# Optimization experiments

Measured on AMD Instinct MI355X. Metric: run time of the kernel, lower is better.

Reference implementation:

```python
import jax, jax.numpy as jnp
import numpy as np

# Module hyper-parameters (match init_kwargs)
WIN = 64        # windowSize -> N
REC = 128       # receptiveSize -> M
H = 8           # numHeads
D = 32          # headDim
DIM = 256       # dim
MAXD = WIN + (REC - WIN) // 2  # maxDisparity = 96

# Static relative position index table, shape (N, M), values in [0, 2*MAXD)
_coords_x = np.arange(WIN)[:, None]
_coords_x_ = (np.arange(REC) - (REC - WIN) // 2)[None, :]
REL_IDX = jnp.asarray(_coords_x - _coords_x_ + MAXD, dtype=jnp.int32)


def setup_inputs() -> dict:
    key = jax.random.key(0)
    ks = jax.random.split(key, 12)
    B, nW = 4, 256
    B_ = B * nW
    x = jax.random.normal(ks[0], (B_, WIN, DIM), jnp.float32)
    x_ = jax.random.normal(ks[1], (B_, REC, DIM), jnp.float32)
    mask_left = jax.random.randint(ks[2], (2, WIN, REC), 0, 2, jnp.int32)
    mask_right = jax.random.randint(ks[3], (2, WIN, REC), 0, 2, jnp.int32)
    s = 0.02
    q_w = jax.random.normal(ks[4], (DIM, H * D), jnp.float32) * s
    q_b = jnp.zeros((H * D,), jnp.float32)
    kv_w = jax.random.normal(ks[5], (DIM, 2 * H * D), jnp.float32) * s
    kv_b = jnp.zeros((2 * H * D,), jnp.float32)
    proj_w = jax.random.normal(ks[6], (H * D, DIM), jnp.float32) * s
    proj_b = jnp.zeros((DIM,), jnp.float32)
    bias_table = jax.random.normal(ks[7], (2 * MAXD, H), jnp.float32) * s
    return dict(x=x, x_=x_, mask_left=mask_left, mask_right=mask_right, nW=nW,
                q_w=q_w, q_b=q_b, kv_w=kv_w, kv_b=kv_b,
                proj_w=proj_w, proj_b=proj_b, bias_table=bias_table)


def reference(x, x_, mask_left, mask_right, nW, q_w, q_b, kv_w, kv_b, proj_w, proj_b, bias_table):
    B_, N, C = x.shape
    M = x_.shape[1]
    B = B_ // nW
    scale = D ** -0.5

    q = (x @ q_w + q_b).reshape(B_, N, H, D).transpose(0, 2, 1, 3)   # b h n d
    kv = x_ @ kv_w + kv_b
    k, v = jnp.split(kv, 2, axis=-1)
    k = k.reshape(B_, M, H, D).transpose(0, 2, 1, 3)                 # b h m d
    v = v.reshape(B_, M, H, D).transpose(0, 2, 1, 3)                 # b h m d

    attn = jnp.einsum('bhnd,bhmd->bhnm', q, k) * scale
    # gathered relative position bias: (N, M, H) -> (H, N, M)
    bias = bias_table[REL_IDX].transpose(2, 0, 1)
    attn = attn + bias[None]

    mask_value = -jnp.finfo(attn.dtype).max
    attn = attn.reshape(B, nW, H, N, M)
    mc = min(mask_left.shape[0], nW)  # static python int
    ml = (mask_left[:mc] == 1)[None, :, None]        # (1, mc, 1, N, M)
    attn = attn.at[:, :mc].set(jnp.where(ml, mask_value, attn[:, :mc]))
    mr = (mask_right[mask_right.shape[0] - mc:] == 1)[None, :, None]
    attn = attn.at[:, nW - mc:].set(jnp.where(mr, mask_value, attn[:, nW - mc:]))
    attn = attn.reshape(B_, H, N, M)

    attn = jax.nn.softmax(attn, axis=-1)
    out = jnp.einsum('bhnm,bhmd->bhnd', attn, v)
    out = out.transpose(0, 2, 1, 3).reshape(B_, N, H * D)
    out = out @ proj_w + proj_b
    return out
```

## Files before the change

### kernel.cpp

```cpp
#include <hip/hip_runtime.h>
#include <float.h>


typedef __attribute__((ext_vector_type(8))) short bf16x8;
typedef __attribute__((ext_vector_type(4))) float f32x4;

static __device__ __forceinline__ unsigned int f2bf(float f) {
    unsigned int u = __float_as_uint(f);
    return (u + 0x7FFFu + ((u >> 16) & 1u)) >> 16;
}
static __device__ __forceinline__ unsigned int pack2(float lo, float hi) {
    return f2bf(lo) | (f2bf(hi) << 16);
}

__device__ unsigned short g_Wt[262144];

__global__ __launch_bounds__(256) void prep_wt(
    const float* __restrict__ q_w, const float* __restrict__ kv_w, const float* __restrict__ proj_w)
{
    const int b = blockIdx.x, k = threadIdx.x;
    float v; unsigned short* dst;
    if (b < 256)      { v = q_w[k * 256 + b];            dst = g_Wt + b * 256; }
    else if (b < 768) { v = kv_w[k * 512 + (b - 256)];   dst = g_Wt + 65536 + (b - 256) * 256; }
    else              { v = proj_w[k * 256 + (b - 768)]; dst = g_Wt + 196608 + (b - 768) * 256; }
    dst[k] = (unsigned short)f2bf(v);
}

template<int NC, int WT_OFF, bool ABF16, bool F32OUT>
__global__ __launch_bounds__(512) void gemm_db(
    const void* __restrict__ Ain, const float* __restrict__ bias, void* __restrict__ Cout)
{
    constexpr int NBN = NC / 128;
    __shared__ __align__(16) unsigned short As[2][128 * 64];
    __shared__ __align__(16) unsigned short Ws[2][128 * 64];

    const int nbx = 8 * NBN;
    const int g = blockIdx.x / nbx, r = blockIdx.x % nbx;
    const int bn = r >> 3, bm = g * 8 + (r & 7);
    const size_t r0 = (size_t)bm * 128;
    const int c0 = bn * 128;

    const int t = threadIdx.x;
    const int wave = t >> 6, lane = t & 63;
    const int lr = lane & 15, hi = lane >> 4;
    const int rw = (wave >> 2) * 64, cw = (wave & 3) * 32;
    const int srow = t >> 2, sks = (t & 3) * 16;
    const int aswz = (srow & 7) << 4;
    const int so1 = (2 * sks) ^ aswz, so2 = (2 * sks + 16) ^ aswz;

    f32x4 acc[4][2];
    #pragma unroll
    for (int i = 0; i < 4; ++i)
        #pragma unroll
        for (int j = 0; j < 2; ++j) acc[i][j] = (f32x4){0.f, 0.f, 0.f, 0.f};

    float4 fA0, fA1, fA2, fA3;
    uint4  sA0, sA1;
    uint4  sW0, sW1;

#define STAGE_LOAD(K0)                                                                     \
    {                                                                                      \
        const unsigned short* wsrc = g_Wt + WT_OFF + (size_t)(c0 + srow) * 256 + (K0) + sks; \
        sW0 = *(const uint4*)wsrc; sW1 = *(const uint4*)(wsrc + 8);                        \
        if (ABF16) {                                                                       \
            const unsigned short* asrc = (const unsigned short*)Ain + (r0 + srow) * 256 + (K0) + sks; \
            sA0 = *(const uint4*)asrc; sA1 = *(const uint4*)(asrc + 8);                    \
        } else {                                                                           \
            const float* asrc = (const float*)Ain + (r0 + srow) * 256 + (K0) + sks;        \
            fA0 = *(const float4*)asrc;       fA1 = *(const float4*)(asrc + 4);            \
            fA2 = *(const float4*)(asrc + 8); fA3 = *(const float4*)(asrc + 12);           \
        }                                                                                  \
    }

#define STAGE_WRITE(B)                                                                     \
    {                                                                                      \
        char* ad = (char*)As[B] + srow * 128;                                              \
        char* wd = (char*)Ws[B] + srow * 128;                                              \
        uint4 u0, u1;                                                                      \
        if (ABF16) { u0 = sA0; u1 = sA1; }                                                 \
        else {                                                                             \
            u0 = make_uint4(pack2(fA0.x, fA0.y), pack2(fA0.z, fA0.w),                      \
                            pack2(fA1.x, fA1.y), pack2(fA1.z, fA1.w));                     \
            u1 = make_uint4(pack2(fA2.x, fA2.y), pack2(fA2.z, fA2.w),                      \
                            pack2(fA3.x, fA3.y), pack2(fA3.z, fA3.w));                     \
        }                                                                                  \
        *(uint4*)(ad + so1) = u0; *(uint4*)(ad + so2) = u1;                                \
        *(uint4*)(wd + so1) = sW0; *(uint4*)(wd + so2) = sW1;                              \
    }

#define COMPUTE(B)                                                                         \
    {                                                                                      \
        const char* Ab = (const char*)As[B];                                               \
        const char* Wb = (const char*)Ws[B];                                               \
        const int swzr = (lr & 7) << 4;                                                    \
        _Pragma("unroll")                                                                  \
        for (int kk = 0; kk < 2; ++kk) {                                                   \
            const int ko = (kk * 64 + hi * 16) ^ swzr;                                     \
            bf16x8 af[4], bf[2];                                                           \
            _Pragma("unroll")                                                              \
            for (int i = 0; i < 4; ++i)                                                    \
                af[i] = *(const bf16x8*)(Ab + (rw + i * 16 + lr) * 128 + ko);              \
            _Pragma("unroll")                                                              \
            for (int j = 0; j < 2; ++j)                                                    \
                bf[j] = *(const bf16x8*)(Wb + (cw + j * 16 + lr) * 128 + ko);              \
            _Pragma("unroll")                                                              \
            for (int i = 0; i < 4; ++i)                                                    \
                _Pragma("unroll")                                                          \
                for (int j = 0; j < 2; ++j)                                                \
                    acc[i][j] = __builtin_amdgcn_mfma_f32_16x16x32_bf16(af[i], bf[j], acc[i][j], 0, 0, 0); \
        }                                                                                  \
    }

    STAGE_LOAD(0); STAGE_WRITE(0); __syncthreads();
    STAGE_LOAD(64);
    COMPUTE(0);
    STAGE_WRITE(1);
    STAGE_LOAD(128);
    __syncthreads();
    COMPUTE(1);
    STAGE_WRITE(0);
    STAGE_LOAD(192);
    __syncthreads();
    COMPUTE(0);
    STAGE_WRITE(1);
    __syncthreads();
    COMPUTE(1);

#undef STAGE_LOAD
#undef STAGE_WRITE
#undef COMPUTE

    #pragma unroll
    for (int i = 0; i < 4; ++i) {
        #pragma unroll
        for (int bj = 0; bj < 2; ++bj) {
            const int col = c0 + cw + bj * 16 + lr;
            const float bb = bias[col];
            #pragma unroll
            for (int q = 0; q < 4; ++q) {
                const size_t row = r0 + rw + i * 16 + 4 * hi + q;
                const float val = acc[i][bj][q] + bb;
                if (F32OUT) ((float*)Cout)[row * NC + col] = val;
                else        ((unsigned short*)Cout)[row * NC + col] = (unsigned short)f2bf(val);
            }
        }
    }
}

__global__ __launch_bounds__(256) void attn_fused(
    const unsigned short* __restrict__ qbf, const unsigned short* __restrict__ kvbf,
    const float* __restrict__ bias_table, const int* __restrict__ mask_left,
    const int* __restrict__ mask_right, unsigned short* __restrict__ aout)
{
    __shared__ __align__(16) unsigned short Qn[64 * 32];
    __shared__ __align__(16) unsigned short Kn[128 * 32];
    __shared__ __align__(16) unsigned short Vt[32 * 128];
    __shared__ __align__(16) unsigned short Pn[64 * 128];
    __shared__ float ballT[8 * 192];

    const int w = blockIdx.x;
    const int t = threadIdx.x;
    const int wave = t >> 6, lane = t & 63;
    const int lr = lane & 15, hi = lane >> 4;
    const int n0w = wave * 16;

    for (int i = t; i < 1536; i += 256) {
        const int hh = i / 192, r = i - hh * 192;
        ballT[i] = bias_table[r * 8 + hh];
    }

    const int wi = w & 255;
    const int* mbase = nullptr;
    if (wi < 2) mbase = mask_left + wi * (64 * 128);
    else if (wi >= 254) mbase = mask_right + (wi - 254) * (64 * 128);

    const float scale = 0.17677669529663687f;

    for (int h = 0; h < 8; ++h) {
        __syncthreads();
        {
            const int n = t >> 2, dq = t & 3;
            const uint4 v = *(const uint4*)(qbf + ((size_t)(w * 64 + n)) * 256 + h * 32 + dq * 8);
            *(uint4*)((char*)Qn + n * 64 + dq * 16) = v;
        }
        #pragma unroll
        for (int i = 0; i < 2; ++i) {
            const int m = (t >> 2) + 64 * i, dq = t & 3;
            const uint4 v = *(const uint4*)(kvbf + ((size_t)(w * 128 + m)) * 512 + h * 32 + dq * 8);
            *(uint4*)((char*)Kn + m * 64 + dq * 16) = v;
        }
        #pragma unroll
        for (int i = 0; i < 2; ++i) {
            const int db = (t >> 7) * 2 + i, m = t & 127;
            const uint4 v = *(const uint4*)(kvbf + ((size_t)(w * 128 + m)) * 512 + 256 + h * 32 + db * 8);
            const unsigned short* vs = (const unsigned short*)&v;
            #pragma unroll
            for (int e = 0; e < 8; ++e) {
                const int d = db * 8 + e;
                *(unsigned short*)((char*)Vt + d * 256 + ((2 * m) ^ ((d & 7) << 4))) = vs[e];
            }
        }
        __syncthreads();

        const bf16x8 qa = *(const bf16x8*)((char*)Qn + (n0w + lr) * 64 + 16 * hi);
        f32x4 sacc[8];
        #pragma unroll
        for (int mj = 0; mj < 8; ++mj) {
            sacc[mj] = (f32x4){0.f, 0.f, 0.f, 0.f};
            const bf16x8 kb = *(const bf16x8*)((char*)Kn + (mj * 16 + lr) * 64 + 16 * hi);
            sacc[mj] = __builtin_amdgcn_mfma_f32_16x16x32_bf16(qa, kb, sacc[mj], 0, 0, 0);
        }

        const float* bh = ballT + h * 192;
        #pragma unroll
        for (int mj = 0; mj < 8; ++mj) {
            const int m = 16 * mj + lr;
            #pragma unroll
            for (int q = 0; q < 4; ++q) {
                const int n = n0w + 4 * hi + q;
                sacc[mj][q] = fmaf(sacc[mj][q], scale, bh[n - m + 128]);
            }
        }
        if (mbase) {
            #pragma unroll
            for (int mj = 0; mj < 8; ++mj) {
                const int m = 16 * mj + lr;
                #pragma unroll
                for (int q = 0; q < 4; ++q) {
                    const int n = n0w + 4 * hi + q;
                    if (mbase[n * 128 + m] == 1) sacc[mj][q] = -FLT_MAX;
                }
            }
        }

        float inv[4];
        #pragma unroll
        for (int q = 0; q < 4; ++q) {
            float mx = sacc[0][q];
            #pragma unroll
            for (int mj = 1; mj < 8; ++mj) mx = fmaxf(mx, sacc[mj][q]);
            mx = fmaxf(mx, __shfl_xor(mx, 1));
            mx = fmaxf(mx, __shfl_xor(mx, 2));
            mx = fmaxf(mx, __shfl_xor(mx, 4));
            mx = fmaxf(mx, __shfl_xor(mx, 8));
            float sm = 0.f;
            #pragma unroll
            for (int mj = 0; mj < 8; ++mj) {
                sacc[mj][q] = __expf(sacc[mj][q] - mx);
                sm += sacc[mj][q];
            }
            sm += __shfl_xor(sm, 1);
            sm += __shfl_xor(sm, 2);
            sm += __shfl_xor(sm, 4);
            sm += __shfl_xor(sm, 8);
            inv[q] = 1.0f / sm;
        }

        #pragma unroll
        for (int mj = 0; mj < 8; ++mj) {
            #pragma unroll
            for (int q = 0; q < 4; ++q) {
                const float pv = sacc[mj][q];
                const float po = __shfl_xor(pv, 1);
                if (!(lane & 1)) {
                    const int n = n0w + 4 * hi + q;
                    const int m = 16 * mj + lr;
                    const unsigned int u = f2bf(pv) | (f2bf(po) << 16);
                    *(unsigned int*)((char*)Pn + n * 256 + ((2 * m) ^ ((n & 7) << 4))) = u;
                }
            }
        }

        f32x4 oacc[2];
        oacc[0] = (f32x4){0.f, 0.f, 0.f, 0.f};
        oacc[1] = (f32x4){0.f, 0.f, 0.f, 0.f};
        const int nA = n0w + lr;
        const int swzA = (nA & 7) << 4;
        #pragma unroll
        for (int kk = 0; kk < 4; ++kk) {
            const bf16x8 pa = *(const bf16x8*)((char*)Pn + nA * 256 + ((64 * kk + 16 * hi) ^ swzA));
            #pragma unroll
            for (int j = 0; j < 2; ++j) {
                const int d = j * 16 + lr;
                const bf16x8 vb = *(const bf16x8*)((char*)Vt + d * 256 + ((64 * kk + 16 * hi) ^ ((d & 7) << 4)));
                oacc[j] = __builtin_amdgcn_mfma_f32_16x16x32_bf16(pa, vb, oacc[j], 0, 0, 0);
            }
        }
        #pragma unroll
        for (int j = 0; j < 2; ++j) {
            #pragma unroll
            for (int q = 0; q < 4; ++q) {
                const int n = n0w + 4 * hi + q;
                aout[((size_t)(w * 64 + n)) * 256 + h * 32 + j * 16 + lr] =
                    (unsigned short)f2bf(oacc[j][q] * inv[q]);
            }
        }
    }
}

extern "C" void kernel_launch(void* const* d_in, const int* in_sizes, int n_in,
                              void* d_out, int out_size, void* d_ws, size_t ws_size,
                              hipStream_t stream)
{
    const float* x      = (const float*)d_in[0];
    const float* x_     = (const float*)d_in[1];
    const int*   mask_l = (const int*)d_in[2];
    const int*   mask_r = (const int*)d_in[3];
    const float* q_w    = (const float*)d_in[5];
    const float* q_b    = (const float*)d_in[6];
    const float* kv_w   = (const float*)d_in[7];
    const float* kv_b   = (const float*)d_in[8];
    const float* proj_w = (const float*)d_in[9];
    const float* proj_b = (const float*)d_in[10];
    const float* bias_t = (const float*)d_in[11];

    unsigned short* qbf  = (unsigned short*)d_ws;
    unsigned short* kvbf = qbf + (size_t)65536 * 256;
    float* out = (float*)d_out;

    prep_wt<<<1024, 256, 0, stream>>>(q_w, kv_w, proj_w);
    gemm_db<256, 0,      false, false><<<1024, 512, 0, stream>>>(x,  q_b,  qbf);
    gemm_db<512, 65536,  false, false><<<4096, 512, 0, stream>>>(x_, kv_b, kvbf);
    attn_fused<<<1024, 256, 0, stream>>>(qbf, kvbf, bias_t, mask_l, mask_r, qbf);
    gemm_db<256, 196608, true,  true ><<<1024, 512, 0, stream>>>(qbf, proj_b, out);
}
```

Baseline: 257.5 us.

## Pre-tile weights into swizzled K-slabs and pipeline GEMM over smaller K-steps

The weight-prep kernel now writes bf16 weights already laid out in the per-block, per-K-slab swizzled order the GEMM uses in shared memory. Each block can then copy a contiguous 8 KB chunk with one coalesced 16-byte load per thread. The GEMM switches from 4 stages of K=64 to 8 stages of K=32 with two loads in flight, halving shared memory per block and adding a 6-blocks-per-CU occupancy hint to improve latency hiding. The cost is more barriers per tile and shorter MFMA runs between synchronisations.

```diff
diff --git a/kernel.cpp b/kernel.cpp
--- a/kernel.cpp
+++ b/kernel.cpp
@@ -18,21 +18,25 @@
 __global__ __launch_bounds__(256) void prep_wt(
     const float* __restrict__ q_w, const float* __restrict__ kv_w, const float* __restrict__ proj_w)
 {
-    const int b = blockIdx.x, k = threadIdx.x;
-    float v; unsigned short* dst;
-    if (b < 256)      { v = q_w[k * 256 + b];            dst = g_Wt + b * 256; }
-    else if (b < 768) { v = kv_w[k * 512 + (b - 256)];   dst = g_Wt + 65536 + (b - 256) * 256; }
-    else              { v = proj_w[k * 256 + (b - 768)]; dst = g_Wt + 196608 + (b - 768) * 256; }
-    dst[k] = (unsigned short)f2bf(v);
+    const int gid = blockIdx.x * 256 + threadIdx.x;
+    int rel, ncs; const float* src;
+    if (gid < 65536)       { rel = gid;          src = q_w;    ncs = 256; }
+    else if (gid < 196608) { rel = gid - 65536;  src = kv_w;   ncs = 512; }
+    else                   { rel = gid - 196608; src = proj_w; ncs = 256; }
+    const int tl = rel >> 12, i = rel & 4095;
+    const int ct = tl >> 3,  ks = tl & 7;
+    const int col = i >> 5,  si = i & 31;
+    const int kl = ((2 * si) ^ ((col & 3) << 4)) >> 1;
+    g_Wt[gid] = (unsigned short)f2bf(src[(ks * 32 + kl) * ncs + ct * 128 + col]);
 }
 
 template<int NC, int WT_OFF, bool ABF16, bool F32OUT>
-__global__ __launch_bounds__(512) void gemm_db(
+__global__ __launch_bounds__(512, 6) void gemm_p(
     const void* __restrict__ Ain, const float* __restrict__ bias, void* __restrict__ Cout)
 {
     constexpr int NBN = NC / 128;
-    __shared__ __align__(16) unsigned short As[2][128 * 64];
-    __shared__ __align__(16) unsigned short Ws[2][128 * 64];
+    __shared__ __align__(16) unsigned short As[2][4096];
+    __shared__ __align__(16) unsigned short Ws[2][4096];
 
     const int nbx = 8 * NBN;
     const int g = blockIdx.x / nbx, r = blockIdx.x % nbx;
@@ -44,9 +48,9 @@
     const int wave = t >> 6, lane = t & 63;
     const int lr = lane & 15, hi = lane >> 4;
     const int rw = (wave >> 2) * 64, cw = (wave & 3) * 32;
-    const int srow = t >> 2, sks = (t & 3) * 16;
-    const int aswz = (srow & 7) << 4;
-    const int so1 = (2 * sks) ^ aswz, so2 = (2 * sks + 16) ^ aswz;
+
+    const int srow = t >> 2, sseg = t & 3;
+    const int aoff = (16 * sseg) ^ ((srow & 3) << 4);
 
     f32x4 acc[4][2];
     #pragma unroll
@@ -54,80 +58,67 @@
         #pragma unroll
         for (int j = 0; j < 2; ++j) acc[i][j] = (f32x4){0.f, 0.f, 0.f, 0.f};
 
-    float4 fA0, fA1, fA2, fA3;
-    uint4  sA0, sA1;
-    uint4  sW0, sW1;
-
-#define STAGE_LOAD(K0)                                                                     \
+    float4 raA[2], raB[2];
+    uint4  rb16[2];
+    uint4  rwv[2];
+
+#define GLOAD(P, S)                                                                        \
     {                                                                                      \
-        const unsigned short* wsrc = g_Wt + WT_OFF + (size_t)(c0 + srow) * 256 + (K0) + sks; \
-        sW0 = *(const uint4*)wsrc; sW1 = *(const uint4*)(wsrc + 8);                        \
+        rwv[P] = *(const uint4*)(g_Wt + WT_OFF + ((size_t)(bn * 8 + (S)) << 12) + t * 8);  \
         if (ABF16) {                                                                       \
-            const unsigned short* asrc = (const unsigned short*)Ain + (r0 + srow) * 256 + (K0) + sks; \
-            sA0 = *(const uint4*)asrc; sA1 = *(const uint4*)(asrc + 8);                    \
+            rb16[P] = *(const uint4*)((const unsigned short*)Ain + (r0 + srow) * 256 + (S) * 32 + sseg * 8); \
         } else {                                                                           \
-            const float* asrc = (const float*)Ain + (r0 + srow) * 256 + (K0) + sks;        \
-            fA0 = *(const float4*)asrc;       fA1 = *(const float4*)(asrc + 4);            \
-            fA2 = *(const float4*)(asrc + 8); fA3 = *(const float4*)(asrc + 12);           \
+            const float* asrc = (const float*)Ain + (r0 + srow) * 256 + (S) * 32 + sseg * 8; \
+            raA[P] = *(const float4*)asrc; raB[P] = *(const float4*)(asrc + 4);            \
         }                                                                                  \
     }
 
-#define STAGE_WRITE(B)                                                                     \
+#define SWRITE(P, B)                                                                       \
     {                                                                                      \
-        char* ad = (char*)As[B] + srow * 128;                                              \
-        char* wd = (char*)Ws[B] + srow * 128;                                              \
-        uint4 u0, u1;                                                                      \
-        if (ABF16) { u0 = sA0; u1 = sA1; }                                                 \
-        else {                                                                             \
-            u0 = make_uint4(pack2(fA0.x, fA0.y), pack2(fA0.z, fA0.w),                      \
-                            pack2(fA1.x, fA1.y), pack2(fA1.z, fA1.w));                     \
-            u1 = make_uint4(pack2(fA2.x, fA2.y), pack2(fA2.z, fA2.w),                      \
-                            pack2(fA3.x, fA3.y), pack2(fA3.z, fA3.w));                     \
-        }                                                                                  \
-        *(uint4*)(ad + so1) = u0; *(uint4*)(ad + so2) = u1;                                \
-        *(uint4*)(wd + so1) = sW0; *(uint4*)(wd + so2) = sW1;                              \
+        uint4 u;                                                                           \
+        if (ABF16) u = rb16[P];                                                            \
+        else u = make_uint4(pack2(raA[P].x, raA[P].y), pack2(raA[P].z, raA[P].w),          \
+                            pack2(raB[P].x, raB[P].y), pack2(raB[P].z, raB[P].w));         \
+        *(uint4*)((char*)As[B] + srow * 64 + aoff) = u;                                    \
+        *(uint4*)((char*)Ws[B] + t * 16) = rwv[P];                                         \
     }
 
 #define COMPUTE(B)                                                                         \
     {                                                                                      \
         const char* Ab = (const char*)As[B];                                               \
         const char* Wb = (const char*)Ws[B];                                               \
-        const int swzr = (lr & 7) << 4;                                                    \
-        _Pragma("unroll")                                                                  \
-        for (int kk = 0; kk < 2; ++kk) {                                                   \
-            const int ko = (kk * 64 + hi * 16) ^ swzr;                                     \
-            bf16x8 af[4], bf[2];                                                           \
-            _Pragma("unroll")                                                              \
-            for (int i = 0; i < 4; ++i)                                                    \
-                af[i] = *(const bf16x8*)(Ab + (rw + i * 16 + lr) * 128 + ko);              \
-            _Pragma("unroll")                                                              \
-            for (int j = 0; j < 2; ++j)                                                    \
-                bf[j] = *(const bf16x8*)(Wb + (cw + j * 16 + lr) * 128 + ko);              \
-            _Pragma("unroll")                                                              \
-            for (int i = 0; i < 4; ++i)                                                    \
-                _Pragma("unroll")                                                          \
-                for (int j = 0; j < 2; ++j)                                                \
-                    acc[i][j] = __builtin_amdgcn_mfma_f32_16x16x32_bf16(af[i], bf[j], acc[i][j], 0, 0, 0); \
-        }                                                                                  \
-    }
-
-    STAGE_LOAD(0); STAGE_WRITE(0); __syncthreads();
-    STAGE_LOAD(64);
-    COMPUTE(0);
-    STAGE_WRITE(1);
-    STAGE_LOAD(128);
+        const int ko = (16 * hi) ^ ((lr & 3) << 4);                                        \
+        bf16x8 af0 = *(const bf16x8*)(Ab + (rw +      lr) * 64 + ko);                      \
+        bf16x8 af1 = *(const bf16x8*)(Ab + (rw + 16 + lr) * 64 + ko);                      \
+        bf16x8 af2 = *(const bf16x8*)(Ab + (rw + 32 + lr) * 64 + ko);                      \
+        bf16x8 af3 = *(const bf16x8*)(Ab + (rw + 48 + lr) * 64 + ko);                      \
+        bf16x8 bg0 = *(const bf16x8*)(Wb + (cw +      lr) * 64 + ko);                      \
+        bf16x8 bg1 = *(const bf16x8*)(Wb + (cw + 16 + lr) * 64 + ko);                      \
+        acc[0][0] = __builtin_amdgcn_mfma_f32_16x16x32_bf16(af0, bg0, acc[0][0], 0, 0, 0); \
+        acc[0][1] = __builtin_amdgcn_mfma_f32_16x16x32_bf16(af0, bg1, acc[0][1], 0, 0, 0); \
+        acc[1][0] = __builtin_amdgcn_mfma_f32_16x16x32_bf16(af1, bg0, acc[1][0], 0, 0, 0); \
+        acc[1][1] = __builtin_amdgcn_mfma_f32_16x16x32_bf16(af1, bg1, acc[1][1], 0, 0, 0); \
+        acc[2][0] = __builtin_amdgcn_mfma_f32_16x16x32_bf16(af2, bg0, acc[2][0], 0, 0, 0); \
+        acc[2][1] = __builtin_amdgcn_mfma_f32_16x16x32_bf16(af2, bg1, acc[2][1], 0, 0, 0); \
+        acc[3][0] = __builtin_amdgcn_mfma_f32_16x16x32_bf16(af3, bg0, acc[3][0], 0, 0, 0); \
+        acc[3][1] = __builtin_amdgcn_mfma_f32_16x16x32_bf16(af3, bg1, acc[3][1], 0, 0, 0); \
+    }
+
+    GLOAD(0, 0); GLOAD(1, 1);
+    SWRITE(0, 0); SWRITE(1, 1);
     __syncthreads();
-    COMPUTE(1);
-    STAGE_WRITE(0);
-    STAGE_LOAD(192);
-    __syncthreads();
-    COMPUTE(0);
-    STAGE_WRITE(1);
-    __syncthreads();
-    COMPUTE(1);
-
-#undef STAGE_LOAD
-#undef STAGE_WRITE
+
+    #pragma unroll 8
+    for (int s = 0; s < 8; ++s) {
+        const int cur = s & 1;
+        if (s < 6) GLOAD(cur, s + 2);
+        COMPUTE(cur);
+        if (s < 7) __syncthreads();
+        if (s < 6) SWRITE(cur, cur);
+    }
+
+#undef GLOAD
+#undef SWRITE
 #undef COMPUTE
 
     #pragma unroll
@@ -319,8 +310,8 @@
     float* out = (float*)d_out;
 
     prep_wt<<<1024, 256, 0, stream>>>(q_w, kv_w, proj_w);
-    gemm_db<256, 0,      false, false><<<1024, 512, 0, stream>>>(x,  q_b,  qbf);
-    gemm_db<512, 65536,  false, false><<<4096, 512, 0, stream>>>(x_, kv_b, kvbf);
+    gemm_p<256, 0,      false, false><<<1024, 512, 0, stream>>>(x,  q_b,  qbf);
+    gemm_p<512, 65536,  false, false><<<4096, 512, 0, stream>>>(x_, kv_b, kvbf);
     attn_fused<<<1024, 256, 0, stream>>>(qbf, kvbf, bias_t, mask_l, mask_r, qbf);
-    gemm_db<256, 196608, true,  true ><<<1024, 512, 0, stream>>>(qbf, proj_b, out);
-}
+    gemm_p<256, 196608, true,  true ><<<1024, 512, 0, stream>>>(qbf, proj_b, out);
+}
```

New measurement: 366.7 us. 42.4% more time.

## Emit V pre-transposed from KV GEMM epilogue to simplify attention loads

Applied to the files above, without the earlier changes.

The KV projection GEMM now writes K and V to separate buffers, with V stored transposed per window (d-major, m contiguous). The attention kernel can then load V into its shared-memory transpose buffer with 16-byte vector copies instead of 8 scalar 2-byte scattered LDS writes per load. This removes the per-element transpose from attention. In exchange, the GEMM epilogue for V does strided 8-byte stores, which may coalesce less well.

```diff
diff --git a/kernel.cpp b/kernel.cpp
--- a/kernel.cpp
+++ b/kernel.cpp
@@ -26,9 +26,10 @@
     dst[k] = (unsigned short)f2bf(v);
 }
 
-template<int NC, int WT_OFF, bool ABF16, bool F32OUT>
+template<int NC, int WT_OFF, bool ABF16, bool F32OUT, bool VSPLIT>
 __global__ __launch_bounds__(512) void gemm_db(
-    const void* __restrict__ Ain, const float* __restrict__ bias, void* __restrict__ Cout)
+    const void* __restrict__ Ain, const float* __restrict__ bias, void* __restrict__ Cout,
+    unsigned short* __restrict__ Vout)
 {
     constexpr int NBN = NC / 128;
     __shared__ __align__(16) unsigned short As[2][128 * 64];
@@ -136,21 +137,36 @@
         for (int bj = 0; bj < 2; ++bj) {
             const int col = c0 + cw + bj * 16 + lr;
             const float bb = bias[col];
-            #pragma unroll
-            for (int q = 0; q < 4; ++q) {
-                const size_t row = r0 + rw + i * 16 + 4 * hi + q;
-                const float val = acc[i][bj][q] + bb;
-                if (F32OUT) ((float*)Cout)[row * NC + col] = val;
-                else        ((unsigned short*)Cout)[row * NC + col] = (unsigned short)f2bf(val);
+            if (VSPLIT && c0 >= 256) {
+                const int vcol = col - 256;
+                const int m0 = rw + i * 16 + 4 * hi;
+                const unsigned int lo = pack2(acc[i][bj][0] + bb, acc[i][bj][1] + bb);
+                const unsigned int h2 = pack2(acc[i][bj][2] + bb, acc[i][bj][3] + bb);
+                *(uint2*)(Vout + (size_t)bm * 32768 + vcol * 128 + m0) = make_uint2(lo, h2);
+            } else if (VSPLIT) {
+                #pragma unroll
+                for (int q = 0; q < 4; ++q) {
+                    const size_t row = r0 + rw + i * 16 + 4 * hi + q;
+                    ((unsigned short*)Cout)[row * 256 + col] = (unsigned short)f2bf(acc[i][bj][q] + bb);
+                }
+            } else {
+                #pragma unroll
+                for (int q = 0; q < 4; ++q) {
+                    const size_t row = r0 + rw + i * 16 + 4 * hi + q;
+                    const float val = acc[i][bj][q] + bb;
+                    if (F32OUT) ((float*)Cout)[row * NC + col] = val;
+                    else        ((unsigned short*)Cout)[row * NC + col] = (unsigned short)f2bf(val);
+                }
             }
         }
     }
 }
 
 __global__ __launch_bounds__(256) void attn_fused(
-    const unsigned short* __restrict__ qbf, const unsigned short* __restrict__ kvbf,
-    const float* __restrict__ bias_table, const int* __restrict__ mask_left,
-    const int* __restrict__ mask_right, unsigned short* __restrict__ aout)
+    const unsigned short* __restrict__ qbf, const unsigned short* __restrict__ kws,
+    const unsigned short* __restrict__ vws, const float* __restrict__ bias_table,
+    const int* __restrict__ mask_left, const int* __restrict__ mask_right,
+    unsigned short* __restrict__ aout)
 {
     __shared__ __align__(16) unsigned short Qn[64 * 32];
     __shared__ __align__(16) unsigned short Kn[128 * 32];
@@ -165,8 +181,8 @@
     const int n0w = wave * 16;
 
     for (int i = t; i < 1536; i += 256) {
-        const int hh = i / 192, r = i - hh * 192;
-        ballT[i] = bias_table[r * 8 + hh];
+        const int hh = i / 192, rr = i - hh * 192;
+        ballT[i] = bias_table[rr * 8 + hh];
     }
 
     const int wi = w & 255;
@@ -186,18 +202,17 @@
         #pragma unroll
         for (int i = 0; i < 2; ++i) {
             const int m = (t >> 2) + 64 * i, dq = t & 3;
-            const uint4 v = *(const uint4*)(kvbf + ((size_t)(w * 128 + m)) * 512 + h * 32 + dq * 8);
+            const uint4 v = *(const uint4*)(kws + ((size_t)(w * 128 + m)) * 256 + h * 32 + dq * 8);
             *(uint4*)((char*)Kn + m * 64 + dq * 16) = v;
         }
-        #pragma unroll
-        for (int i = 0; i < 2; ++i) {
-            const int db = (t >> 7) * 2 + i, m = t & 127;
-            const uint4 v = *(const uint4*)(kvbf + ((size_t)(w * 128 + m)) * 512 + 256 + h * 32 + db * 8);
-            const unsigned short* vs = (const unsigned short*)&v;
-            #pragma unroll
-            for (int e = 0; e < 8; ++e) {
-                const int d = db * 8 + e;
-                *(unsigned short*)((char*)Vt + d * 256 + ((2 * m) ^ ((d & 7) << 4))) = vs[e];
+        {
+            const unsigned short* vsrc = vws + (size_t)w * 32768 + h * 32 * 128;
+            #pragma unroll
+            for (int i = 0; i < 2; ++i) {
+                const int u = t + i * 256;
+                const int d = u >> 4, mseg = u & 15;
+                const uint4 vv = *(const uint4*)(vsrc + d * 128 + mseg * 8);
+                *(uint4*)((char*)Vt + d * 256 + ((mseg * 16) ^ ((d & 7) << 4))) = vv;
             }
         }
         __syncthreads();
@@ -265,8 +280,8 @@
                 if (!(lane & 1)) {
                     const int n = n0w + 4 * hi + q;
                     const int m = 16 * mj + lr;
-                    const unsigned int u = f2bf(pv) | (f2bf(po) << 16);
-                    *(unsigned int*)((char*)Pn + n * 256 + ((2 * m) ^ ((n & 7) << 4))) = u;
+                    *(unsigned int*)((char*)Pn + n * 256 + ((2 * m) ^ ((n & 7) << 4))) =
+                        f2bf(pv) | (f2bf(po) << 16);
                 }
             }
         }
@@ -314,13 +329,14 @@
     const float* proj_b = (const float*)d_in[10];
     const float* bias_t = (const float*)d_in[11];
 
-    unsigned short* qbf  = (unsigned short*)d_ws;
-    unsigned short* kvbf = qbf + (size_t)65536 * 256;
+    unsigned short* qbf = (unsigned short*)d_ws;
+    unsigned short* kws = qbf + (size_t)65536 * 256;
+    unsigned short* vws = kws + (size_t)131072 * 256;
     float* out = (float*)d_out;
 
     prep_wt<<<1024, 256, 0, stream>>>(q_w, kv_w, proj_w);
-    gemm_db<256, 0,      false, false><<<1024, 512, 0, stream>>>(x,  q_b,  qbf);
-    gemm_db<512, 65536,  false, false><<<4096, 512, 0, stream>>>(x_, kv_b, kvbf);
-    attn_fused<<<1024, 256, 0, stream>>>(qbf, kvbf, bias_t, mask_l, mask_r, qbf);
-    gemm_db<256, 196608, true,  true ><<<1024, 512, 0, stream>>>(qbf, proj_b, out);
-}
+    gemm_db<256, 0,      false, false, false><<<1024, 512, 0, stream>>>(x,  q_b,  qbf, nullptr);
+    gemm_db<512, 65536,  false, false, true ><<<4096, 512, 0, stream>>>(x_, kv_b, kws, vws);
+    attn_fused<<<1024, 256, 0, stream>>>(qbf, kws, vws, bias_t, mask_l, mask_r, qbf);
+    gemm_db<256, 196608, true,  true,  false><<<1024, 512, 0, stream>>>(qbf, proj_b, out, nullptr);
+}
```

Result: slower. 265.4 us (+3.1%).
